# Kernel tuning notes

Measured on AMD Instinct MI355X. Metric: run time of the kernel, lower is better.

The kernel has to match this reference:

```python
import jax, jax.numpy as jnp
import numpy as np

INPUT_DIM = 1024
OUT_DIM = 1024
ORDER = 4
EXPANSION_POINT = 0.0


def setup_inputs() -> dict:
    key = jax.random.key(0)
    k_x, k_c = jax.random.split(key)
    x = jax.random.normal(k_x, (8192, INPUT_DIM), dtype=jnp.float32)
    coeffs = jax.random.normal(k_c, (OUT_DIM, INPUT_DIM, ORDER), dtype=jnp.float32) * 0.01
    bias = jnp.zeros((1, OUT_DIM), dtype=jnp.float32)
    return {"x": x, "coeffs": coeffs, "bias": bias}


def reference(x, coeffs, bias):
    # x: [..., input_dim] -> flatten leading dims
    outshape = x.shape[:-1] + (OUT_DIM,)
    xf = x.reshape(-1, INPUT_DIM)
    x_shifted = xf - EXPANSION_POINT
    # powers P[n, i, k] = x_shifted^k, k = 0..order-1 (0**0 == 1, matching torch)
    powers = jnp.power(x_shifted[:, :, None], jnp.arange(ORDER, dtype=x.dtype))
    # y[n, o] = sum_{i,k} P[n,i,k] * coeffs[o,i,k]  -- single GEMM-like contraction
    y = jnp.einsum('nik,oik->no', powers, coeffs)
    y = y + bias
    return y.reshape(outshape)
```

## Files before the change

### kernel.cpp

```cpp
#include <hip/hip_runtime.h>
#include <stdint.h>

#define IN_DIM 1024
#define OUT_DIM 1024
#define NROWS 8192
#define KD 3072

#define BM 256
#define BN 128
#define BK 64
#define NT (KD / BK)

typedef __bf16 bf16x8 __attribute__((ext_vector_type(8)));
typedef float f32x4 __attribute__((ext_vector_type(4)));
typedef unsigned short us8 __attribute__((ext_vector_type(8)));
typedef unsigned int u32;

#define AS1 __attribute__((address_space(1)))
#define AS3 __attribute__((address_space(3)))

__device__ __forceinline__ unsigned short f2bf(float f) {
    u32 u = __builtin_bit_cast(u32, f);
    u32 r = (u + 0x7fffu + ((u >> 16) & 1u)) >> 16;
    return (unsigned short)r;
}

__device__ __forceinline__ bf16x8 ld8(const unsigned short* p) {
    return __builtin_bit_cast(bf16x8, *reinterpret_cast<const us8*>(p));
}

__global__ __launch_bounds__(256) void prep_coeffs(const float* __restrict__ c,
                                                   const float* __restrict__ bias,
                                                   unsigned short* __restrict__ B,
                                                   float* __restrict__ bias2) {
    const int o = blockIdx.x;
    const float4* row = reinterpret_cast<const float4*>(c + (size_t)o * (IN_DIM * 4));
    unsigned short* Bo = B + (size_t)o * KD;
    float s = 0.f;
    for (int i = threadIdx.x; i < IN_DIM; i += 256) {
        float4 v = row[i];
        s += v.x;
        Bo[i]        = f2bf(v.y);
        Bo[1024 + i] = f2bf(v.z);
        Bo[2048 + i] = f2bf(v.w);
    }
#pragma unroll
    for (int off = 32; off; off >>= 1) s += __shfl_down(s, off);
    __shared__ float red[4];
    if ((threadIdx.x & 63) == 0) red[threadIdx.x >> 6] = s;
    __syncthreads();
    if (threadIdx.x == 0) bias2[o] = bias[o] + red[0] + red[1] + red[2] + red[3];
}

__global__ __launch_bounds__(256) void prep_powers(const float* __restrict__ x,
                                                   unsigned short* __restrict__ A) {
    int t = blockIdx.x * blockDim.x + threadIdx.x;
    int n = t >> 8;
    int i4 = (t & 255) * 4;
    float4 v = reinterpret_cast<const float4*>(x)[t];
    unsigned short* An = A + (size_t)n * KD + i4;
    float xs[4] = {v.x, v.y, v.z, v.w};
    unsigned short b1[4], b2[4], b3[4];
#pragma unroll
    for (int j = 0; j < 4; ++j) {
        float x1 = xs[j], x2 = x1 * x1, x3 = x2 * x1;
        b1[j] = f2bf(x1); b2[j] = f2bf(x2); b3[j] = f2bf(x3);
    }
    ushort4 p1 = {b1[0], b1[1], b1[2], b1[3]};
    ushort4 p2 = {b2[0], b2[1], b2[2], b2[3]};
    ushort4 p3 = {b3[0], b3[1], b3[2], b3[3]};
    *reinterpret_cast<ushort4*>(An)        = p1;
    *reinterpret_cast<ushort4*>(An + 1024) = p2;
    *reinterpret_cast<ushort4*>(An + 2048) = p3;
}

__global__ __launch_bounds__(512, 1) void taylor_gemm(
    const unsigned short* __restrict__ A,
    const unsigned short* __restrict__ B,
    const float* __restrict__ bias2,
    float* __restrict__ C) {
    __shared__ alignas(16) unsigned short sA[3][BM * BK];
    __shared__ alignas(16) unsigned short sB[3][BN * BK];

    const int tid = threadIdx.x;
    const int lane = tid & 63;
    const int wid = tid >> 6;
    const int wr = wid >> 2;
    const int wc = wid & 3;
    const int gx = blockIdx.x, gy = blockIdx.y;

    const char* Ab = (const char*)A;
    const char* Bb = (const char*)B;
    const int cs = ((lane & 7) ^ (lane >> 3)) * 8;
    size_t aSrc[4], bSrc[2];
    int aDst[4], bDst[2];
#pragma unroll
    for (int u = 0; u < 4; ++u) {
        int row = gx * BM + u * 64 + wid * 8 + (lane >> 3);
        aSrc[u] = ((size_t)row * KD + cs) * 2;
        aDst[u] = (u * 64 + wid * 8) * BK;
    }
#pragma unroll
    for (int u = 0; u < 2; ++u) {
        int row = gy * BN + u * 64 + wid * 8 + (lane >> 3);
        bSrc[u] = ((size_t)row * KD + cs) * 2;
        bDst[u] = (u * 64 + wid * 8) * BK;
    }

    auto stage_unit = [&](int b, int kt, int u) {
        size_t koff = (size_t)kt * (BK * 2);
        if (u < 4)
            __builtin_amdgcn_global_load_lds(
                (const AS1 void*)(Ab + aSrc[u] + koff),
                (AS3 void*)(&sA[b][aDst[u]]), 16, 0, 0);
        else
            __builtin_amdgcn_global_load_lds(
                (const AS1 void*)(Bb + bSrc[u - 4] + koff),
                (AS3 void*)(&sB[b][bDst[u - 4]]), 16, 0, 0);
    };

    int aSw[2], bSw[2];
#pragma unroll
    for (int ks = 0; ks < 2; ++ks) {
        int sw = ((ks * 4 + (lane >> 4)) ^ (lane & 7)) * 8;
        aSw[ks] = (wr * 128 + (lane & 15)) * BK + sw;
        bSw[ks] = (wc * 32 + (lane & 15)) * BK + sw;
    }

    f32x4 acc[8][2] = {};

#pragma unroll
    for (int u = 0; u < 6; ++u) stage_unit(0, 0, u);
#pragma unroll
    for (int u = 0; u < 6; ++u) stage_unit(1, 1, u);

    for (int kt = 0; kt < NT; ++kt) {
        const int cb = kt % 3;
        const int nb = (kt + 2) % 3;
        if (kt < NT - 1) asm volatile("s_waitcnt vmcnt(6)" ::: "memory");
        else             asm volatile("s_waitcnt vmcnt(0)" ::: "memory");
        __builtin_amdgcn_s_barrier();
        __builtin_amdgcn_sched_barrier(0);

        const unsigned short* sAc = &sA[cb][0];
        const unsigned short* sBc = &sB[cb][0];
        const bool doStage = (kt < NT - 2);

        bf16x8 bf[2][2], af[4][2];
#pragma unroll
        for (int n = 0; n < 2; ++n)
#pragma unroll
            for (int ks = 0; ks < 2; ++ks)
                bf[n][ks] = ld8(&sBc[bSw[ks] + n * 16 * BK]);
#pragma unroll
        for (int mi = 0; mi < 4; ++mi)
#pragma unroll
            for (int ks = 0; ks < 2; ++ks)
                af[mi][ks] = ld8(&sAc[aSw[ks] + mi * 16 * BK]);
        if (doStage) {
            stage_unit(nb, kt + 2, 0);
            stage_unit(nb, kt + 2, 4);
            stage_unit(nb, kt + 2, 1);
        }
        asm volatile("s_waitcnt lgkmcnt(0)" ::: "memory");
        __builtin_amdgcn_sched_barrier(0);
        __builtin_amdgcn_s_setprio(1);
#pragma unroll
        for (int mi = 0; mi < 4; ++mi)
#pragma unroll
            for (int n = 0; n < 2; ++n)
#pragma unroll
                for (int ks = 0; ks < 2; ++ks)
                    acc[mi][n] = __builtin_amdgcn_mfma_f32_16x16x32_bf16(
                        af[mi][ks], bf[n][ks], acc[mi][n], 0, 0, 0);
        __builtin_amdgcn_s_setprio(0);
        __builtin_amdgcn_s_barrier();
        __builtin_amdgcn_sched_barrier(0);

        bf16x8 af2[4][2];
#pragma unroll
        for (int mi = 0; mi < 4; ++mi)
#pragma unroll
            for (int ks = 0; ks < 2; ++ks)
                af2[mi][ks] = ld8(&sAc[aSw[ks] + (4 + mi) * 16 * BK]);
        if (doStage) {
            stage_unit(nb, kt + 2, 5);
            stage_unit(nb, kt + 2, 2);
            stage_unit(nb, kt + 2, 3);
        }
        asm volatile("s_waitcnt lgkmcnt(0)" ::: "memory");
        __builtin_amdgcn_sched_barrier(0);
        __builtin_amdgcn_s_setprio(1);
#pragma unroll
        for (int mi = 0; mi < 4; ++mi)
#pragma unroll
            for (int n = 0; n < 2; ++n)
#pragma unroll
                for (int ks = 0; ks < 2; ++ks)
                    acc[4 + mi][n] = __builtin_amdgcn_mfma_f32_16x16x32_bf16(
                        af2[mi][ks], bf[n][ks], acc[4 + mi][n], 0, 0, 0);
        __builtin_amdgcn_s_setprio(0);
        __builtin_amdgcn_s_barrier();
        __builtin_amdgcn_sched_barrier(0);
    }

    const int colBase = gy * BN + wc * 32 + (lane & 15);
    const int rowBase = gx * BM + wr * 128 + (lane >> 4) * 4;
#pragma unroll
    for (int n = 0; n < 2; ++n) {
        int col = colBase + n * 16;
        float bv = bias2[col];
#pragma unroll
        for (int m = 0; m < 8; ++m) {
            int row = rowBase + m * 16;
#pragma unroll
            for (int r = 0; r < 4; ++r)
                C[(size_t)(row + r) * OUT_DIM + col] = acc[m][n][r] + bv;
        }
    }
}

__global__ void taylor_naive(const float* __restrict__ x, const float* __restrict__ coeffs,
                             const float* __restrict__ bias, float* __restrict__ out) {
    int n = blockIdx.x;
    __shared__ float P[IN_DIM * 4];
    for (int i = threadIdx.x; i < IN_DIM; i += blockDim.x) {
        float xv = x[(size_t)n * IN_DIM + i];
        P[i * 4 + 0] = 1.f;
        P[i * 4 + 1] = xv;
        P[i * 4 + 2] = xv * xv;
        P[i * 4 + 3] = xv * xv * xv;
    }
    __syncthreads();
    for (int o = threadIdx.x; o < OUT_DIM; o += blockDim.x) {
        float s = bias[o];
        const float* c = coeffs + (size_t)o * (IN_DIM * 4);
        for (int i = 0; i < IN_DIM; ++i) {
            float4 cv = *reinterpret_cast<const float4*>(c + i * 4);
            s += cv.x * P[i * 4 + 0] + cv.y * P[i * 4 + 1] +
                 cv.z * P[i * 4 + 2] + cv.w * P[i * 4 + 3];
        }
        out[(size_t)n * OUT_DIM + o] = s;
    }
}

extern "C" void kernel_launch(void* const* d_in, const int* in_sizes, int n_in,
                              void* d_out, int out_size, void* d_ws, size_t ws_size,
                              hipStream_t stream) {
    const float* x = (const float*)d_in[0];
    const float* coeffs = (const float*)d_in[1];
    const float* bias = (const float*)d_in[2];
    float* out = (float*)d_out;

    const size_t needA = (size_t)NROWS * KD * 2;
    const size_t needB = (size_t)OUT_DIM * KD * 2;
    const size_t needBias = OUT_DIM * sizeof(float);

    if (ws_size >= needA + needB + needBias) {
        unsigned short* A = (unsigned short*)d_ws;
        unsigned short* B = (unsigned short*)((char*)d_ws + needA);
        float* bias2 = (float*)((char*)d_ws + needA + needB);
        prep_coeffs<<<OUT_DIM, 256, 0, stream>>>(coeffs, bias, B, bias2);
        prep_powers<<<(NROWS * IN_DIM / 4) / 256, 256, 0, stream>>>(x, A);
        dim3 grid(NROWS / BM, OUT_DIM / BN);
        taylor_gemm<<<grid, 512, 0, stream>>>(A, B, bias2, out);
    } else {
        taylor_naive<<<NROWS, 256, 0, stream>>>(x, coeffs, bias, out);
    }
}
```

Baseline: 75.53 us.

## Use 256x256 GEMM tiles with split-K over two halves and atomic accumulation

Fuses the two prep kernels into one launch and widens the GEMM output tile from 256x128 to 256x256, which halves the number of times each A tile is loaded. The K dimension is split in two across blockIdx.z, and partial sums are combined with float atomicAdd into an output zeroed by a memset. Buffering drops from triple to double, and the loads are reorganised into four MFMA phases per k-step. The cost is an extra memset, atomic write traffic at 2x the output size, and a shallower prefetch pipeline; the summation order across the two halves is also no longer fixed.

```diff
diff --git a/kernel.cpp b/kernel.cpp
--- a/kernel.cpp
+++ b/kernel.cpp
@@ -5,11 +5,12 @@
 #define OUT_DIM 1024
 #define NROWS 8192
 #define KD 3072
+#define KHALF 1536
 
 #define BM 256
-#define BN 128
+#define BN 256
 #define BK 64
-#define NT (KD / BK)
+#define NTH (KHALF / BK)
 
 typedef __bf16 bf16x8 __attribute__((ext_vector_type(8)));
 typedef float f32x4 __attribute__((ext_vector_type(4)));
@@ -29,49 +30,50 @@
     return __builtin_bit_cast(bf16x8, *reinterpret_cast<const us8*>(p));
 }
 
-__global__ __launch_bounds__(256) void prep_coeffs(const float* __restrict__ c,
+__global__ __launch_bounds__(256) void taylor_prep(const float* __restrict__ x,
+                                                   const float* __restrict__ c,
                                                    const float* __restrict__ bias,
+                                                   unsigned short* __restrict__ A,
                                                    unsigned short* __restrict__ B,
                                                    float* __restrict__ bias2) {
-    const int o = blockIdx.x;
-    const float4* row = reinterpret_cast<const float4*>(c + (size_t)o * (IN_DIM * 4));
-    unsigned short* Bo = B + (size_t)o * KD;
-    float s = 0.f;
-    for (int i = threadIdx.x; i < IN_DIM; i += 256) {
-        float4 v = row[i];
-        s += v.x;
-        Bo[i]        = f2bf(v.y);
-        Bo[1024 + i] = f2bf(v.z);
-        Bo[2048 + i] = f2bf(v.w);
-    }
-#pragma unroll
-    for (int off = 32; off; off >>= 1) s += __shfl_down(s, off);
-    __shared__ float red[4];
-    if ((threadIdx.x & 63) == 0) red[threadIdx.x >> 6] = s;
-    __syncthreads();
-    if (threadIdx.x == 0) bias2[o] = bias[o] + red[0] + red[1] + red[2] + red[3];
-}
-
-__global__ __launch_bounds__(256) void prep_powers(const float* __restrict__ x,
-                                                   unsigned short* __restrict__ A) {
-    int t = blockIdx.x * blockDim.x + threadIdx.x;
-    int n = t >> 8;
-    int i4 = (t & 255) * 4;
-    float4 v = reinterpret_cast<const float4*>(x)[t];
-    unsigned short* An = A + (size_t)n * KD + i4;
-    float xs[4] = {v.x, v.y, v.z, v.w};
-    unsigned short b1[4], b2[4], b3[4];
-#pragma unroll
-    for (int j = 0; j < 4; ++j) {
-        float x1 = xs[j], x2 = x1 * x1, x3 = x2 * x1;
-        b1[j] = f2bf(x1); b2[j] = f2bf(x2); b3[j] = f2bf(x3);
-    }
-    ushort4 p1 = {b1[0], b1[1], b1[2], b1[3]};
-    ushort4 p2 = {b2[0], b2[1], b2[2], b2[3]};
-    ushort4 p3 = {b3[0], b3[1], b3[2], b3[3]};
-    *reinterpret_cast<ushort4*>(An)        = p1;
-    *reinterpret_cast<ushort4*>(An + 1024) = p2;
-    *reinterpret_cast<ushort4*>(An + 2048) = p3;
+    if (blockIdx.x < 8192) {
+        int t = blockIdx.x * 256 + threadIdx.x;
+        int n = t >> 8;
+        int i4 = (t & 255) * 4;
+        float4 v = reinterpret_cast<const float4*>(x)[t];
+        unsigned short* An = A + (size_t)n * KD + i4;
+        float xs[4] = {v.x, v.y, v.z, v.w};
+        unsigned short b1[4], b2[4], b3[4];
+#pragma unroll
+        for (int j = 0; j < 4; ++j) {
+            float x1 = xs[j], x2 = x1 * x1, x3 = x2 * x1;
+            b1[j] = f2bf(x1); b2[j] = f2bf(x2); b3[j] = f2bf(x3);
+        }
+        ushort4 p1 = {b1[0], b1[1], b1[2], b1[3]};
+        ushort4 p2 = {b2[0], b2[1], b2[2], b2[3]};
+        ushort4 p3 = {b3[0], b3[1], b3[2], b3[3]};
+        *reinterpret_cast<ushort4*>(An)        = p1;
+        *reinterpret_cast<ushort4*>(An + 1024) = p2;
+        *reinterpret_cast<ushort4*>(An + 2048) = p3;
+    } else {
+        const int o = blockIdx.x - 8192;
+        const float4* row = reinterpret_cast<const float4*>(c + (size_t)o * (IN_DIM * 4));
+        unsigned short* Bo = B + (size_t)o * KD;
+        float s = 0.f;
+        for (int i = threadIdx.x; i < IN_DIM; i += 256) {
+            float4 v = row[i];
+            s += v.x;
+            Bo[i]        = f2bf(v.y);
+            Bo[1024 + i] = f2bf(v.z);
+            Bo[2048 + i] = f2bf(v.w);
+        }
+#pragma unroll
+        for (int off = 32; off; off >>= 1) s += __shfl_down(s, off);
+        __shared__ float red[4];
+        if ((threadIdx.x & 63) == 0) red[threadIdx.x >> 6] = s;
+        __syncthreads();
+        if (threadIdx.x == 0) bias2[o] = bias[o] + red[0] + red[1] + red[2] + red[3];
+    }
 }
 
 __global__ __launch_bounds__(512, 1) void taylor_gemm(
@@ -79,89 +81,77 @@
     const unsigned short* __restrict__ B,
     const float* __restrict__ bias2,
     float* __restrict__ C) {
-    __shared__ alignas(16) unsigned short sA[3][BM * BK];
-    __shared__ alignas(16) unsigned short sB[3][BN * BK];
+    __shared__ alignas(16) unsigned short sA[2][BM * BK];
+    __shared__ alignas(16) unsigned short sB[2][BN * BK];
 
     const int tid = threadIdx.x;
     const int lane = tid & 63;
     const int wid = tid >> 6;
     const int wr = wid >> 2;
     const int wc = wid & 3;
-    const int gx = blockIdx.x, gy = blockIdx.y;
+    const int gx = blockIdx.x, gy = blockIdx.y, kz = blockIdx.z;
 
     const char* Ab = (const char*)A;
     const char* Bb = (const char*)B;
     const int cs = ((lane & 7) ^ (lane >> 3)) * 8;
-    size_t aSrc[4], bSrc[2];
-    int aDst[4], bDst[2];
+    const size_t kzoff = (size_t)kz * KHALF * 2;
+    size_t aSrc[4], bSrc[4];
+    int uDst[4];
 #pragma unroll
     for (int u = 0; u < 4; ++u) {
-        int row = gx * BM + u * 64 + wid * 8 + (lane >> 3);
-        aSrc[u] = ((size_t)row * KD + cs) * 2;
-        aDst[u] = (u * 64 + wid * 8) * BK;
-    }
-#pragma unroll
-    for (int u = 0; u < 2; ++u) {
-        int row = gy * BN + u * 64 + wid * 8 + (lane >> 3);
-        bSrc[u] = ((size_t)row * KD + cs) * 2;
-        bDst[u] = (u * 64 + wid * 8) * BK;
-    }
-
-    auto stage_unit = [&](int b, int kt, int u) {
-        size_t koff = (size_t)kt * (BK * 2);
-        if (u < 4)
-            __builtin_amdgcn_global_load_lds(
-                (const AS1 void*)(Ab + aSrc[u] + koff),
-                (AS3 void*)(&sA[b][aDst[u]]), 16, 0, 0);
-        else
-            __builtin_amdgcn_global_load_lds(
-                (const AS1 void*)(Bb + bSrc[u - 4] + koff),
-                (AS3 void*)(&sB[b][bDst[u - 4]]), 16, 0, 0);
+        int rrow = u * 64 + wid * 8 + (lane >> 3);
+        aSrc[u] = ((size_t)(gx * BM + rrow) * KD + cs) * 2 + kzoff;
+        bSrc[u] = ((size_t)(gy * BN + rrow) * KD + cs) * 2 + kzoff;
+        uDst[u] = (u * 64 + wid * 8) * BK;
+    }
+
+    auto stage_A = [&](int b, int kt, int u) {
+        __builtin_amdgcn_global_load_lds(
+            (const AS1 void*)(Ab + aSrc[u] + (size_t)kt * (BK * 2)),
+            (AS3 void*)(&sA[b][uDst[u]]), 16, 0, 0);
     };
-
-    int aSw[2], bSw[2];
+    auto stage_B = [&](int b, int kt, int u) {
+        __builtin_amdgcn_global_load_lds(
+            (const AS1 void*)(Bb + bSrc[u] + (size_t)kt * (BK * 2)),
+            (AS3 void*)(&sB[b][uDst[u]]), 16, 0, 0);
+    };
+
+    int aBase[2], bBase[2];
 #pragma unroll
     for (int ks = 0; ks < 2; ++ks) {
         int sw = ((ks * 4 + (lane >> 4)) ^ (lane & 7)) * 8;
-        aSw[ks] = (wr * 128 + (lane & 15)) * BK + sw;
-        bSw[ks] = (wc * 32 + (lane & 15)) * BK + sw;
-    }
-
-    f32x4 acc[8][2] = {};
-
-#pragma unroll
-    for (int u = 0; u < 6; ++u) stage_unit(0, 0, u);
-#pragma unroll
-    for (int u = 0; u < 6; ++u) stage_unit(1, 1, u);
-
-    for (int kt = 0; kt < NT; ++kt) {
-        const int cb = kt % 3;
-        const int nb = (kt + 2) % 3;
-        if (kt < NT - 1) asm volatile("s_waitcnt vmcnt(6)" ::: "memory");
-        else             asm volatile("s_waitcnt vmcnt(0)" ::: "memory");
-        __builtin_amdgcn_s_barrier();
-        __builtin_amdgcn_sched_barrier(0);
-
-        const unsigned short* sAc = &sA[cb][0];
-        const unsigned short* sBc = &sB[cb][0];
-        const bool doStage = (kt < NT - 2);
-
-        bf16x8 bf[2][2], af[4][2];
+        aBase[ks] = (wr * 128 + (lane & 15)) * BK + sw;
+        bBase[ks] = (wc * 64 + (lane & 15)) * BK + sw;
+    }
+
+    f32x4 acc[8][4] = {};
+
+    stage_B(0, 0, 0); stage_B(0, 0, 1); stage_B(0, 0, 2); stage_B(0, 0, 3);
+    stage_A(0, 0, 0); stage_A(0, 0, 2); stage_A(0, 0, 1); stage_A(0, 0, 3);
+    asm volatile("s_waitcnt vmcnt(2)" ::: "memory");
+    __builtin_amdgcn_s_barrier();
+    __builtin_amdgcn_sched_barrier(0);
+
+    for (int kt = 0; kt < NTH; ++kt) {
+        const int d = kt & 1, nd = d ^ 1;
+        const bool doStage = (kt + 1 < NTH);
+        const unsigned short* sAc = &sA[d][0];
+        const unsigned short* sBc = &sB[d][0];
+
+        bf16x8 bf01[2][2], bf23[2][2], af03[4][2], af47[4][2];
+
+#pragma unroll
+        for (int mi = 0; mi < 4; ++mi)
+#pragma unroll
+            for (int ks = 0; ks < 2; ++ks)
+                af03[mi][ks] = ld8(&sAc[aBase[ks] + mi * 16 * BK]);
 #pragma unroll
         for (int n = 0; n < 2; ++n)
 #pragma unroll
             for (int ks = 0; ks < 2; ++ks)
-                bf[n][ks] = ld8(&sBc[bSw[ks] + n * 16 * BK]);
-#pragma unroll
-        for (int mi = 0; mi < 4; ++mi)
-#pragma unroll
-            for (int ks = 0; ks < 2; ++ks)
-                af[mi][ks] = ld8(&sAc[aSw[ks] + mi * 16 * BK]);
-        if (doStage) {
-            stage_unit(nb, kt + 2, 0);
-            stage_unit(nb, kt + 2, 4);
-            stage_unit(nb, kt + 2, 1);
-        }
+                bf01[n][ks] = ld8(&sBc[bBase[ks] + n * 16 * BK]);
+        if (doStage) { stage_B(nd, kt + 1, 0); stage_B(nd, kt + 1, 1); }
+        __builtin_amdgcn_s_barrier();
         asm volatile("s_waitcnt lgkmcnt(0)" ::: "memory");
         __builtin_amdgcn_sched_barrier(0);
         __builtin_amdgcn_s_setprio(1);
@@ -172,22 +162,18 @@
 #pragma unroll
                 for (int ks = 0; ks < 2; ++ks)
                     acc[mi][n] = __builtin_amdgcn_mfma_f32_16x16x32_bf16(
-                        af[mi][ks], bf[n][ks], acc[mi][n], 0, 0, 0);
-        __builtin_amdgcn_s_setprio(0);
-        __builtin_amdgcn_s_barrier();
-        __builtin_amdgcn_sched_barrier(0);
-
-        bf16x8 af2[4][2];
-#pragma unroll
-        for (int mi = 0; mi < 4; ++mi)
-#pragma unroll
-            for (int ks = 0; ks < 2; ++ks)
-                af2[mi][ks] = ld8(&sAc[aSw[ks] + (4 + mi) * 16 * BK]);
-        if (doStage) {
-            stage_unit(nb, kt + 2, 5);
-            stage_unit(nb, kt + 2, 2);
-            stage_unit(nb, kt + 2, 3);
-        }
+                        af03[mi][ks], bf01[n][ks], acc[mi][n], 0, 0, 0);
+        __builtin_amdgcn_s_setprio(0);
+        __builtin_amdgcn_s_barrier();
+        __builtin_amdgcn_sched_barrier(0);
+
+#pragma unroll
+        for (int n = 0; n < 2; ++n)
+#pragma unroll
+            for (int ks = 0; ks < 2; ++ks)
+                bf23[n][ks] = ld8(&sBc[bBase[ks] + (2 + n) * 16 * BK]);
+        if (doStage) { stage_B(nd, kt + 1, 2); stage_B(nd, kt + 1, 3); }
+        __builtin_amdgcn_s_barrier();
         asm volatile("s_waitcnt lgkmcnt(0)" ::: "memory");
         __builtin_amdgcn_sched_barrier(0);
         __builtin_amdgcn_s_setprio(1);
@@ -197,25 +183,66 @@
             for (int n = 0; n < 2; ++n)
 #pragma unroll
                 for (int ks = 0; ks < 2; ++ks)
+                    acc[mi][2 + n] = __builtin_amdgcn_mfma_f32_16x16x32_bf16(
+                        af03[mi][ks], bf23[n][ks], acc[mi][2 + n], 0, 0, 0);
+        __builtin_amdgcn_s_setprio(0);
+        if (doStage) asm volatile("s_waitcnt vmcnt(4)" ::: "memory");
+        else         asm volatile("s_waitcnt vmcnt(0)" ::: "memory");
+        __builtin_amdgcn_s_barrier();
+        __builtin_amdgcn_sched_barrier(0);
+
+#pragma unroll
+        for (int mi = 0; mi < 4; ++mi)
+#pragma unroll
+            for (int ks = 0; ks < 2; ++ks)
+                af47[mi][ks] = ld8(&sAc[aBase[ks] + (4 + mi) * 16 * BK]);
+        if (doStage) { stage_A(nd, kt + 1, 0); stage_A(nd, kt + 1, 2); }
+        __builtin_amdgcn_s_barrier();
+        asm volatile("s_waitcnt lgkmcnt(0)" ::: "memory");
+        __builtin_amdgcn_sched_barrier(0);
+        __builtin_amdgcn_s_setprio(1);
+#pragma unroll
+        for (int mi = 0; mi < 4; ++mi)
+#pragma unroll
+            for (int n = 0; n < 2; ++n)
+#pragma unroll
+                for (int ks = 0; ks < 2; ++ks)
+                    acc[4 + mi][2 + n] = __builtin_amdgcn_mfma_f32_16x16x32_bf16(
+                        af47[mi][ks], bf23[n][ks], acc[4 + mi][2 + n], 0, 0, 0);
+        __builtin_amdgcn_s_setprio(0);
+        __builtin_amdgcn_s_barrier();
+        __builtin_amdgcn_sched_barrier(0);
+
+        if (doStage) { stage_A(nd, kt + 1, 1); stage_A(nd, kt + 1, 3); }
+        __builtin_amdgcn_s_barrier();
+        __builtin_amdgcn_s_setprio(1);
+#pragma unroll
+        for (int mi = 0; mi < 4; ++mi)
+#pragma unroll
+            for (int n = 0; n < 2; ++n)
+#pragma unroll
+                for (int ks = 0; ks < 2; ++ks)
                     acc[4 + mi][n] = __builtin_amdgcn_mfma_f32_16x16x32_bf16(
-                        af2[mi][ks], bf[n][ks], acc[4 + mi][n], 0, 0, 0);
-        __builtin_amdgcn_s_setprio(0);
-        __builtin_amdgcn_s_barrier();
-        __builtin_amdgcn_sched_barrier(0);
-    }
-
-    const int colBase = gy * BN + wc * 32 + (lane & 15);
+                        af47[mi][ks], bf01[n][ks], acc[4 + mi][n], 0, 0, 0);
+        __builtin_amdgcn_s_setprio(0);
+        if (doStage) asm volatile("s_waitcnt vmcnt(2)" ::: "memory");
+        else         asm volatile("s_waitcnt vmcnt(0)" ::: "memory");
+        __builtin_amdgcn_s_barrier();
+        __builtin_amdgcn_sched_barrier(0);
+    }
+
+    const int colBase = gy * BN + wc * 64 + (lane & 15);
     const int rowBase = gx * BM + wr * 128 + (lane >> 4) * 4;
 #pragma unroll
-    for (int n = 0; n < 2; ++n) {
+    for (int n = 0; n < 4; ++n) {
         int col = colBase + n * 16;
-        float bv = bias2[col];
+        float bv = (kz == 0) ? bias2[col] : 0.f;
 #pragma unroll
         for (int m = 0; m < 8; ++m) {
             int row = rowBase + m * 16;
 #pragma unroll
             for (int r = 0; r < 4; ++r)
-                C[(size_t)(row + r) * OUT_DIM + col] = acc[m][n][r] + bv;
+                atomicAdd(&C[(size_t)(row + r) * OUT_DIM + col], acc[m][n][r] + bv);
         }
     }
 }
@@ -260,9 +287,9 @@
         unsigned short* A = (unsigned short*)d_ws;
         unsigned short* B = (unsigned short*)((char*)d_ws + needA);
         float* bias2 = (float*)((char*)d_ws + needA + needB);
-        prep_coeffs<<<OUT_DIM, 256, 0, stream>>>(coeffs, bias, B, bias2);
-        prep_powers<<<(NROWS * IN_DIM / 4) / 256, 256, 0, stream>>>(x, A);
-        dim3 grid(NROWS / BM, OUT_DIM / BN);
+        hipMemsetAsync(out, 0, (size_t)out_size * sizeof(float), stream);
+        taylor_prep<<<8192 + 1024, 256, 0, stream>>>(x, coeffs, bias, A, B, bias2);
+        dim3 grid(NROWS / BM, OUT_DIM / BN, 2);
         taylor_gemm<<<grid, 512, 0, stream>>>(A, B, bias2, out);
     } else {
         taylor_naive<<<NROWS, 256, 0, stream>>>(x, coeffs, bias, out);
```

Result: slower. 118.0 us (+56.3%).
